# Kernel tuning notes

Hardware: AMD Instinct MI355X
Metric: run time of the kernel (lower is better)

Reference implementation:

```python
import jax, jax.numpy as jnp
import numpy as np

B, S, D = 2, 4096, 768
H, HD = 12, 64  # num_head, head_dim


def setup_inputs() -> dict:
    key = jax.random.key(0)
    ks = jax.random.split(key, 10)
    s = 0.02
    return {
        "X": jax.random.normal(ks[0], (B, S, D), dtype=jnp.float32),
        "mask": jnp.ones((B, S), dtype=jnp.float32),
        "Wq": jax.random.normal(ks[1], (D, H * HD), dtype=jnp.float32) * s,
        "bq": jnp.zeros((H * HD,), dtype=jnp.float32),
        "Wk": jax.random.normal(ks[2], (D, H * HD), dtype=jnp.float32) * s,
        "bk": jnp.zeros((H * HD,), dtype=jnp.float32),
        "Wv": jax.random.normal(ks[3], (D, H * HD), dtype=jnp.float32) * s,
        "bv": jnp.zeros((H * HD,), dtype=jnp.float32),
        "Wo": jax.random.normal(ks[4], (H * HD, D), dtype=jnp.float32) * s,
        "bo": jnp.zeros((D,), dtype=jnp.float32),
    }


def _split_heads(x):
    # [B,S,H*HD] -> [B,H,S,HD]
    return x.reshape(B, S, H, HD).transpose(0, 2, 1, 3)


def reference(X, mask, Wq, bq, Wk, bk, Wv, bv, Wo, bo):
    Q = _split_heads(X @ Wq + bq)
    K = _split_heads(X @ Wk + bk)
    V = _split_heads(X @ Wv + bv)
    # scores: [B,H,S,S]
    dot = jnp.einsum("bhqd,bhkd->bhqk", Q, K) / np.sqrt(HD).astype(np.float32)
    dot = dot - 1e6 * (1.0 - mask[:, None, None, :])
    attn = jax.nn.softmax(dot, axis=-1)
    ctx = jnp.einsum("bhqk,bhkd->bhqd", attn, V)
    # combine heads: [B,H,S,HD] -> [B,S,H*HD]
    ctx = ctx.transpose(0, 2, 1, 3).reshape(B, S, H * HD)
    return ctx @ Wo + bo
```

## Files before the change

### kernel.cpp

```cpp
#include <hip/hip_runtime.h>

#define BATCH   2
#define S_LEN   4096
#define D_MODEL 768
#define NH      12
#define HDIM    64
#define MROWS   (BATCH * S_LEN)
#define QBLK    128
#define KVBLK   64
#define NT      (S_LEN / KVBLK)
#define LOG2E   1.4426950408889634f

typedef float f32x4  __attribute__((ext_vector_type(4)));
typedef float f32x16 __attribute__((ext_vector_type(16)));
typedef short bf16x8 __attribute__((ext_vector_type(8)));

#if __has_builtin(__builtin_amdgcn_exp2f)
#define EXP2(x) __builtin_amdgcn_exp2f(x)
#else
#define EXP2(x) exp2f(x)
#endif

static __device__ __forceinline__ unsigned short f2bf(float f) {
  union { float f; unsigned u; } v; v.f = f;
  unsigned r = v.u + 0x7fffu + ((v.u >> 16) & 1u);
  return (unsigned short)(r >> 16);
}

static __device__ __forceinline__ unsigned cvtpk(float lo, float hi) {
  unsigned r;
  asm("v_cvt_pk_bf16_f32 %0, %1, %2" : "=v"(r) : "v"(lo), "v"(hi));
  return r;
}

typedef __attribute__((address_space(1))) const unsigned int as1_cuint;
typedef __attribute__((address_space(3))) unsigned int as3_uint;
static __device__ __forceinline__ void gload_lds16(const unsigned short* g,
                                                   unsigned short* l) {
  __builtin_amdgcn_global_load_lds((as1_cuint*)g, (as3_uint*)l, 16, 0, 0);
}

template <int BASE>
static __device__ __forceinline__ bf16x8 pack_frag(const f32x16& s) {
  unsigned a0 = cvtpk(s[BASE + 0], s[BASE + 1]);
  unsigned b0 = cvtpk(s[BASE + 4], s[BASE + 5]);
  asm("v_permlane32_swap_b32 %0, %1" : "+v"(a0), "+v"(b0));
  unsigned a1 = cvtpk(s[BASE + 2], s[BASE + 3]);
  unsigned b1 = cvtpk(s[BASE + 6], s[BASE + 7]);
  asm("v_permlane32_swap_b32 %0, %1" : "+v"(a1), "+v"(b1));
  union { unsigned w[4]; bf16x8 v; } u;
  u.w[0] = a0; u.w[1] = a1; u.w[2] = b0; u.w[3] = b1;
  return u.v;
}

#define Z16 {0.f,0.f,0.f,0.f,0.f,0.f,0.f,0.f,0.f,0.f,0.f,0.f,0.f,0.f,0.f,0.f}


__global__ void conv_x(const float* __restrict__ X, unsigned short* __restrict__ Xb) {
  int i = blockIdx.x * blockDim.x + threadIdx.x;
  float4 v = ((const float4*)X)[i];
  ushort4 o;
  o.x = f2bf(v.x); o.y = f2bf(v.y); o.z = f2bf(v.z); o.w = f2bf(v.w);
  ((ushort4*)Xb)[i] = o;
}

__global__ __launch_bounds__(1024) void mask_prep(const float* __restrict__ mask,
                                                  float* __restrict__ madd,
                                                  int* __restrict__ flag) {
  __shared__ int ok[16];
  int t = threadIdx.x;
  int all1 = 1;
  #pragma unroll
  for (int i = 0; i < MROWS / 1024; ++i) {
    int idx = i * 1024 + t;
    float m = mask[idx];
    madd[idx] = (-1e6f * LOG2E) * (1.0f - m);
    all1 &= (m == 1.0f);
  }
  all1 = __all(all1) ? 1 : 0;
  if ((t & 63) == 0) ok[t >> 6] = all1;
  __syncthreads();
  if (t == 0) {
    int a = 1;
    #pragma unroll
    for (int i = 0; i < 16; ++i) a &= ok[i];
    *flag = a;
  }
}

__global__ __launch_bounds__(256) void trans_w(
    const float* __restrict__ W0, const float* __restrict__ W1,
    const float* __restrict__ W2, const float* __restrict__ W3,
    unsigned short* __restrict__ T0, unsigned short* __restrict__ T1,
    unsigned short* __restrict__ T2, unsigned short* __restrict__ T3) {
  const float* W; unsigned short* T;
  int zz = blockIdx.z;
  if (zz == 0) { W = W0; T = T0; }
  else if (zz == 1) { W = W1; T = T1; }
  else if (zz == 2) { W = W2; T = T2; }
  else { W = W3; T = T3; }
  __shared__ float tile[32][33];
  int tx = threadIdx.x & 31, ty = threadIdx.x >> 5;
  int bx = blockIdx.x * 32, by = blockIdx.y * 32;
  #pragma unroll
  for (int i = ty; i < 32; i += 8) tile[i][tx] = W[(size_t)(by + i) * D_MODEL + bx + tx];
  __syncthreads();
  #pragma unroll
  for (int i = ty; i < 32; i += 8)
    T[(size_t)(bx + i) * D_MODEL + by + tx] = f2bf(tile[tx][i]);
}

__global__ __launch_bounds__(256) void qkv_gemm(
    const unsigned short* __restrict__ Xb,
    const unsigned short* __restrict__ Wqt, const unsigned short* __restrict__ Wkt,
    const unsigned short* __restrict__ Wvt,
    const float* __restrict__ bq, const float* __restrict__ bk, const float* __restrict__ bv,
    unsigned short* __restrict__ Qo, unsigned short* __restrict__ Ko,
    unsigned short* __restrict__ Vto) {
  __shared__ unsigned short As[128 * 64];
  __shared__ unsigned short Bs[128 * 64];
  int zz = blockIdx.z;
  const unsigned short* Wt = zz == 0 ? Wqt : (zz == 1 ? Wkt : Wvt);
  const float* bias = zz == 0 ? bq : (zz == 1 ? bk : bv);
  int tid = threadIdx.x;
  int w = tid >> 6, lane = tid & 63, lr = lane & 15, lg = lane >> 4;
  int wr = w >> 1, wc = w & 1;
  int mb = blockIdx.x * 128, nb = blockIdx.y * 128;
  const unsigned short* Ag = Xb + (size_t)(mb + (tid >> 3)) * D_MODEL + (tid & 7) * 8;
  const unsigned short* Bg = Wt + (size_t)(nb + (tid >> 3)) * D_MODEL + (tid & 7) * 8;
  unsigned short* Al = As + (size_t)tid * 8;
  unsigned short* Bl = Bs + (size_t)tid * 8;
  f32x4 acc[4][4];
  #pragma unroll
  for (int m = 0; m < 4; ++m)
    #pragma unroll
    for (int n = 0; n < 4; ++n) acc[m][n] = (f32x4){0.f, 0.f, 0.f, 0.f};
  for (int kb = 0; kb < D_MODEL / 64; ++kb) {
    __syncthreads();
    #pragma unroll
    for (int i = 0; i < 4; ++i) {
      gload_lds16(Ag + (size_t)(i * 32) * D_MODEL + kb * 64, Al + i * 2048);
      gload_lds16(Bg + (size_t)(i * 32) * D_MODEL + kb * 64, Bl + i * 2048);
    }
    __syncthreads();
    #pragma unroll
    for (int kk = 0; kk < 2; ++kk) {
      bf16x8 af[4], bfv[4];
      #pragma unroll
      for (int m = 0; m < 4; ++m)
        af[m] = *(const bf16x8*)(As + (wr * 64 + m * 16 + lr) * 64 + kk * 32 + lg * 8);
      #pragma unroll
      for (int n = 0; n < 4; ++n)
        bfv[n] = *(const bf16x8*)(Bs + (wc * 64 + n * 16 + lr) * 64 + kk * 32 + lg * 8);
      #pragma unroll
      for (int m = 0; m < 4; ++m)
        #pragma unroll
        for (int n = 0; n < 4; ++n)
          acc[m][n] = __builtin_amdgcn_mfma_f32_16x16x32_bf16(af[m], bfv[n], acc[m][n], 0, 0, 0);
    }
  }
  #pragma unroll
  for (int n = 0; n < 4; ++n) {
    int nc = nb + wc * 64 + n * 16 + lr;
    float bia = bias[nc];
    int h = nc >> 6, hd = nc & 63;
    #pragma unroll
    for (int m = 0; m < 4; ++m) {
      #pragma unroll
      for (int r = 0; r < 4; ++r) {
        int mr = mb + wr * 64 + m * 16 + lg * 4 + r;
        int b = mr >> 12, s = mr & 4095;
        float val = acc[m][n][r] + bia;
        if (zz == 0)
          Qo[((size_t)(b * NH + h) * S_LEN + s) * HDIM + hd] = f2bf(val * 0.125f * LOG2E);
        else if (zz == 1)
          Ko[((size_t)(b * NH + h) * S_LEN + s) * HDIM + hd] = f2bf(val);
        else
          Vto[((size_t)(b * NH + h) * HDIM + hd) * S_LEN + s] = f2bf(val);
      }
    }
  }
}

__global__ __launch_bounds__(256) void attn_kernel(
    const unsigned short* __restrict__ Q, const unsigned short* __restrict__ K,
    const unsigned short* __restrict__ Vt, const float* __restrict__ madd,
    const int* __restrict__ allones_p, unsigned short* __restrict__ Ctx) {
  __shared__ unsigned short Ks[2][64][72];
  __shared__ unsigned short Vs[2][64][72];
  int lin = blockIdx.x;
  int wg = (lin & 7) * 96 + (lin >> 3);
  int qb = wg & 31, bh = wg >> 5;
  int b = bh / NH, h = bh % NH;
  int tid = threadIdx.x;
  int w = tid >> 6, lane = tid & 63;
  int lq = lane & 31, hi = lane >> 5;
  const unsigned short* Qb = Q + (size_t)bh * S_LEN * HDIM;
  const unsigned short* Kb = K + (size_t)bh * S_LEN * HDIM;
  const unsigned short* Vb = Vt + (size_t)bh * HDIM * S_LEN;
  const float* maddb = madd + (size_t)b * S_LEN;
  const int allones = *allones_p;

  int qrow = qb * QBLK + w * 32 + lq;
  bf16x8 qf0 = *(const bf16x8*)(Qb + (size_t)qrow * HDIM + 0 * 16 + hi * 8);
  bf16x8 qf1 = *(const bf16x8*)(Qb + (size_t)qrow * HDIM + 1 * 16 + hi * 8);
  bf16x8 qf2 = *(const bf16x8*)(Qb + (size_t)qrow * HDIM + 2 * 16 + hi * 8);
  bf16x8 qf3 = *(const bf16x8*)(Qb + (size_t)qrow * HDIM + 3 * 16 + hi * 8);

  f32x16 acc0 = Z16, acc1 = Z16;
  float l_run = 0.f;

  int srow = tid >> 3, sseg = (tid & 7) * 8;
  uint4 ka, kc, va, vc;

  ka = *(const uint4*)(Kb + (size_t)srow * HDIM + sseg);
  kc = *(const uint4*)(Kb + (size_t)(srow + 32) * HDIM + sseg);
  va = *(const uint4*)(Vb + (size_t)srow * S_LEN + sseg);
  vc = *(const uint4*)(Vb + (size_t)(srow + 32) * S_LEN + sseg);
  *(uint4*)&Ks[0][srow][sseg]      = ka;
  *(uint4*)&Ks[0][srow + 32][sseg] = kc;
  *(uint4*)&Vs[0][srow][sseg]      = va;
  *(uint4*)&Vs[0][srow + 32][sseg] = vc;
  __syncthreads();

  for (int t = 0; t < NT; ++t) {
    int cur = t & 1;
    int kbase = t * KVBLK;
    if (t + 1 < NT) {
      int nb2 = kbase + KVBLK;
      ka = *(const uint4*)(Kb + (size_t)(nb2 + srow) * HDIM + sseg);
      kc = *(const uint4*)(Kb + (size_t)(nb2 + srow + 32) * HDIM + sseg);
      va = *(const uint4*)(Vb + (size_t)srow * S_LEN + nb2 + sseg);
      vc = *(const uint4*)(Vb + (size_t)(srow + 32) * S_LEN + nb2 + sseg);
    }
    f32x16 s0 = Z16, s1 = Z16;
    #pragma unroll
    for (int c = 0; c < 4; ++c) {
      bf16x8 kf0 = *(const bf16x8*)(&Ks[cur][lq][c * 16 + hi * 8]);
      bf16x8 kf1 = *(const bf16x8*)(&Ks[cur][32 + lq][c * 16 + hi * 8]);
      bf16x8 qf = c == 0 ? qf0 : (c == 1 ? qf1 : (c == 2 ? qf2 : qf3));
      s0 = __builtin_amdgcn_mfma_f32_32x32x16_bf16(kf0, qf, s0, 0, 0, 0);
      s1 = __builtin_amdgcn_mfma_f32_32x32x16_bf16(kf1, qf, s1, 0, 0, 0);
    }
    if (!allones) {
      #pragma unroll
      for (int g = 0; g < 4; ++g) {
        float4 m0 = *(const float4*)(maddb + kbase + g * 8 + hi * 4);
        float4 m1 = *(const float4*)(maddb + kbase + 32 + g * 8 + hi * 4);
        s0[g * 4 + 0] += m0.x; s0[g * 4 + 1] += m0.y;
        s0[g * 4 + 2] += m0.z; s0[g * 4 + 3] += m0.w;
        s1[g * 4 + 0] += m1.x; s1[g * 4 + 1] += m1.y;
        s1[g * 4 + 2] += m1.z; s1[g * 4 + 3] += m1.w;
      }
    }
    float psA = 0.f, psB = 0.f, psC = 0.f, psD = 0.f;
    #pragma unroll
    for (int r = 0; r < 4; ++r) {
      s0[r]      = EXP2(s0[r]);      psA += s0[r];
      s0[r + 4]  = EXP2(s0[r + 4]);  psB += s0[r + 4];
      s0[r + 8]  = EXP2(s0[r + 8]);  psC += s0[r + 8];
      s0[r + 12] = EXP2(s0[r + 12]); psD += s0[r + 12];
    }
    #pragma unroll
    for (int r = 0; r < 4; ++r) {
      s1[r]      = EXP2(s1[r]);      psA += s1[r];
      s1[r + 4]  = EXP2(s1[r + 4]);  psB += s1[r + 4];
      s1[r + 8]  = EXP2(s1[r + 8]);  psC += s1[r + 8];
      s1[r + 12] = EXP2(s1[r + 12]); psD += s1[r + 12];
    }
    float psum = (psA + psB) + (psC + psD);
    psum += __shfl_xor(psum, 32, 64);
    l_run += psum;
    bf16x8 pa0 = pack_frag<0>(s0);
    bf16x8 pa1 = pack_frag<8>(s0);
    bf16x8 pa2 = pack_frag<0>(s1);
    bf16x8 pa3 = pack_frag<8>(s1);
    #pragma unroll
    for (int c = 0; c < 4; ++c) {
      bf16x8 pa = c == 0 ? pa0 : (c == 1 ? pa1 : (c == 2 ? pa2 : pa3));
      bf16x8 vf0 = *(const bf16x8*)(&Vs[cur][lq][c * 16 + hi * 8]);
      bf16x8 vf1 = *(const bf16x8*)(&Vs[cur][32 + lq][c * 16 + hi * 8]);
      acc0 = __builtin_amdgcn_mfma_f32_32x32x16_bf16(pa, vf0, acc0, 0, 0, 0);
      acc1 = __builtin_amdgcn_mfma_f32_32x32x16_bf16(pa, vf1, acc1, 0, 0, 0);
    }
    if (t + 1 < NT) {
      int nxt = cur ^ 1;
      *(uint4*)&Ks[nxt][srow][sseg]      = ka;
      *(uint4*)&Ks[nxt][srow + 32][sseg] = kc;
      *(uint4*)&Vs[nxt][srow][sseg]      = va;
      *(uint4*)&Vs[nxt][srow + 32][sseg] = vc;
      __syncthreads();
    }
  }
  #pragma unroll
  for (int r = 0; r < 16; ++r) {
    int qr = (r & 3) + 8 * (r >> 2) + 4 * hi;
    float lv = __shfl(l_run, qr, 64);
    float rl = 1.0f / lv;
    int qglob = qb * QBLK + w * 32 + qr;
    size_t base = ((size_t)(b * S_LEN + qglob)) * D_MODEL + h * HDIM;
    Ctx[base + lq]      = f2bf(acc0[r] * rl);
    Ctx[base + 32 + lq] = f2bf(acc1[r] * rl);
  }
}

__global__ __launch_bounds__(256) void out_gemm(
    const unsigned short* __restrict__ Ctx, const unsigned short* __restrict__ Wot,
    const float* __restrict__ bo, float* __restrict__ Out) {
  __shared__ unsigned short As[128 * 64];
  __shared__ unsigned short Bs[128 * 64];
  int tid = threadIdx.x;
  int w = tid >> 6, lane = tid & 63, lr = lane & 15, lg = lane >> 4;
  int wr = w >> 1, wc = w & 1;
  int mb = blockIdx.x * 128, nb = blockIdx.y * 128;
  const unsigned short* Ag = Ctx + (size_t)(mb + (tid >> 3)) * D_MODEL + (tid & 7) * 8;
  const unsigned short* Bg = Wot + (size_t)(nb + (tid >> 3)) * D_MODEL + (tid & 7) * 8;
  unsigned short* Al = As + (size_t)tid * 8;
  unsigned short* Bl = Bs + (size_t)tid * 8;
  f32x4 acc[4][4];
  #pragma unroll
  for (int m = 0; m < 4; ++m)
    #pragma unroll
    for (int n = 0; n < 4; ++n) acc[m][n] = (f32x4){0.f, 0.f, 0.f, 0.f};
  for (int kb = 0; kb < D_MODEL / 64; ++kb) {
    __syncthreads();
    #pragma unroll
    for (int i = 0; i < 4; ++i) {
      gload_lds16(Ag + (size_t)(i * 32) * D_MODEL + kb * 64, Al + i * 2048);
      gload_lds16(Bg + (size_t)(i * 32) * D_MODEL + kb * 64, Bl + i * 2048);
    }
    __syncthreads();
    #pragma unroll
    for (int kk = 0; kk < 2; ++kk) {
      bf16x8 af[4], bfv[4];
      #pragma unroll
      for (int m = 0; m < 4; ++m)
        af[m] = *(const bf16x8*)(As + (wr * 64 + m * 16 + lr) * 64 + kk * 32 + lg * 8);
      #pragma unroll
      for (int n = 0; n < 4; ++n)
        bfv[n] = *(const bf16x8*)(Bs + (wc * 64 + n * 16 + lr) * 64 + kk * 32 + lg * 8);
      #pragma unroll
      for (int m = 0; m < 4; ++m)
        #pragma unroll
        for (int n = 0; n < 4; ++n)
          acc[m][n] = __builtin_amdgcn_mfma_f32_16x16x32_bf16(af[m], bfv[n], acc[m][n], 0, 0, 0);
    }
  }
  #pragma unroll
  for (int n = 0; n < 4; ++n) {
    int nc = nb + wc * 64 + n * 16 + lr;
    float bia = bo[nc];
    #pragma unroll
    for (int m = 0; m < 4; ++m) {
      #pragma unroll
      for (int r = 0; r < 4; ++r) {
        int mr = mb + wr * 64 + m * 16 + lg * 4 + r;
        Out[(size_t)mr * D_MODEL + nc] = acc[m][n][r] + bia;
      }
    }
  }
}


extern "C" void kernel_launch(void* const* d_in, const int* in_sizes, int n_in,
                              void* d_out, int out_size, void* d_ws, size_t ws_size,
                              hipStream_t stream) {
  const float* X    = (const float*)d_in[0];
  const float* mask = (const float*)d_in[1];
  const float* Wq   = (const float*)d_in[2];
  const float* bq   = (const float*)d_in[3];
  const float* Wk   = (const float*)d_in[4];
  const float* bk   = (const float*)d_in[5];
  const float* Wv   = (const float*)d_in[6];
  const float* bv   = (const float*)d_in[7];
  const float* Wo   = (const float*)d_in[8];
  const float* bo   = (const float*)d_in[9];
  float* out = (float*)d_out;
  char* ws = (char*)d_ws;

  const size_t XB_OFF   = 0;
  const size_t WQT_OFF  = 12582912;
  const size_t WKT_OFF  = WQT_OFF + 1179648;
  const size_t WVT_OFF  = WKT_OFF + 1179648;
  const size_t WOT_OFF  = WVT_OFF + 1179648;
  const size_t Q_OFF    = WOT_OFF + 1179648;
  const size_t K_OFF    = Q_OFF + 12582912;
  const size_t VT_OFF   = K_OFF + 12582912;
  const size_t CTX_OFF  = VT_OFF + 12582912;
  const size_t MADD_OFF = CTX_OFF + 12582912;
  const size_t FLAG_OFF = MADD_OFF + MROWS * 4;

  unsigned short* Xb  = (unsigned short*)(ws + XB_OFF);
  unsigned short* Wqt = (unsigned short*)(ws + WQT_OFF);
  unsigned short* Wkt = (unsigned short*)(ws + WKT_OFF);
  unsigned short* Wvt = (unsigned short*)(ws + WVT_OFF);
  unsigned short* Wot = (unsigned short*)(ws + WOT_OFF);
  unsigned short* Qw  = (unsigned short*)(ws + Q_OFF);
  unsigned short* Kw  = (unsigned short*)(ws + K_OFF);
  unsigned short* Vtw = (unsigned short*)(ws + VT_OFF);
  unsigned short* Ctx = (unsigned short*)(ws + CTX_OFF);
  float* madd = (float*)(ws + MADD_OFF);
  int* flag   = (int*)(ws + FLAG_OFF);

  conv_x<<<dim3(MROWS * D_MODEL / 4 / 256), 256, 0, stream>>>(X, Xb);
  mask_prep<<<dim3(1), 1024, 0, stream>>>(mask, madd, flag);
  trans_w<<<dim3(24, 24, 4), 256, 0, stream>>>(Wq, Wk, Wv, Wo, Wqt, Wkt, Wvt, Wot);
  qkv_gemm<<<dim3(MROWS / 128, D_MODEL / 128, 3), 256, 0, stream>>>(
      Xb, Wqt, Wkt, Wvt, bq, bk, bv, Qw, Kw, Vtw);
  attn_kernel<<<dim3((S_LEN / QBLK) * (BATCH * NH)), 256, 0, stream>>>(
      Qw, Kw, Vtw, madd, flag, Ctx);
  out_gemm<<<dim3(MROWS / 128, D_MODEL / 128), 256, 0, stream>>>(Ctx, Wot, bo, out);
}
```

Measured before the change: 257.6 us.

## Split attention KV range in two halves and merge with combine kernel

Splits each attention workgroup's KV sweep into two halves processed by separate workgroups, doubling the grid from 768 to 1536 blocks. Each half writes unnormalized bf16 partial outputs and row sums, and a new combine kernel adds the partials and divides by the summed denominators. The aim is better occupancy and load balance across the GPU's compute units. In exchange it adds an extra kernel launch, extra global traffic, and extra bf16 rounding of unnormalized partials, and it reuses the Xb and weight-transpose buffers as scratch. It relies on the absence of a running max, so partial sums add directly.

New measurement: 260.7 us. About the same (+1.2%).

```diff
diff --git a/kernel.cpp b/kernel.cpp
--- a/kernel.cpp
+++ b/kernel.cpp
@@ -8,7 +8,8 @@
 #define MROWS   (BATCH * S_LEN)
 #define QBLK    128
 #define KVBLK   64
-#define NT      (S_LEN / KVBLK)
+#define KVHALF  2048
+#define NTH     (KVHALF / KVBLK)
 #define LOG2E   1.4426950408889634f
 
 typedef float f32x4  __attribute__((ext_vector_type(4)));
@@ -25,6 +26,10 @@
   union { float f; unsigned u; } v; v.f = f;
   unsigned r = v.u + 0x7fffu + ((v.u >> 16) & 1u);
   return (unsigned short)(r >> 16);
+}
+
+static __device__ __forceinline__ float bf2f(unsigned short u) {
+  union { unsigned u; float f; } v; v.u = ((unsigned)u) << 16; return v.f;
 }
 
 static __device__ __forceinline__ unsigned cvtpk(float lo, float hi) {
@@ -185,12 +190,17 @@
 __global__ __launch_bounds__(256) void attn_kernel(
     const unsigned short* __restrict__ Q, const unsigned short* __restrict__ K,
     const unsigned short* __restrict__ Vt, const float* __restrict__ madd,
-    const int* __restrict__ allones_p, unsigned short* __restrict__ Ctx) {
+    const int* __restrict__ allones_p,
+    unsigned short* __restrict__ OutA, unsigned short* __restrict__ OutB,
+    float* __restrict__ lA, float* __restrict__ lB) {
   __shared__ unsigned short Ks[2][64][72];
   __shared__ unsigned short Vs[2][64][72];
   int lin = blockIdx.x;
-  int wg = (lin & 7) * 96 + (lin >> 3);
-  int qb = wg & 31, bh = wg >> 5;
+  int wg = (lin & 7) * 192 + (lin >> 3);
+  int bh = wg >> 6;
+  int rem = wg & 63;
+  int half = rem & 1;
+  int qb = rem >> 1;
   int b = bh / NH, h = bh % NH;
   int tid = threadIdx.x;
   int w = tid >> 6, lane = tid & 63;
@@ -200,6 +210,8 @@
   const unsigned short* Vb = Vt + (size_t)bh * HDIM * S_LEN;
   const float* maddb = madd + (size_t)b * S_LEN;
   const int allones = *allones_p;
+  unsigned short* outp = half ? OutB : OutA;
+  float* lp = half ? lB : lA;
 
   int qrow = qb * QBLK + w * 32 + lq;
   bf16x8 qf0 = *(const bf16x8*)(Qb + (size_t)qrow * HDIM + 0 * 16 + hi * 8);
@@ -211,22 +223,23 @@
   float l_run = 0.f;
 
   int srow = tid >> 3, sseg = (tid & 7) * 8;
+  int kv0 = half * KVHALF;
   uint4 ka, kc, va, vc;
 
-  ka = *(const uint4*)(Kb + (size_t)srow * HDIM + sseg);
-  kc = *(const uint4*)(Kb + (size_t)(srow + 32) * HDIM + sseg);
-  va = *(const uint4*)(Vb + (size_t)srow * S_LEN + sseg);
-  vc = *(const uint4*)(Vb + (size_t)(srow + 32) * S_LEN + sseg);
+  ka = *(const uint4*)(Kb + (size_t)(kv0 + srow) * HDIM + sseg);
+  kc = *(const uint4*)(Kb + (size_t)(kv0 + srow + 32) * HDIM + sseg);
+  va = *(const uint4*)(Vb + (size_t)srow * S_LEN + kv0 + sseg);
+  vc = *(const uint4*)(Vb + (size_t)(srow + 32) * S_LEN + kv0 + sseg);
   *(uint4*)&Ks[0][srow][sseg]      = ka;
   *(uint4*)&Ks[0][srow + 32][sseg] = kc;
   *(uint4*)&Vs[0][srow][sseg]      = va;
   *(uint4*)&Vs[0][srow + 32][sseg] = vc;
   __syncthreads();
 
-  for (int t = 0; t < NT; ++t) {
+  for (int t = 0; t < NTH; ++t) {
     int cur = t & 1;
-    int kbase = t * KVBLK;
-    if (t + 1 < NT) {
+    int kbase = kv0 + t * KVBLK;
+    if (t + 1 < NTH) {
       int nb2 = kbase + KVBLK;
       ka = *(const uint4*)(Kb + (size_t)(nb2 + srow) * HDIM + sseg);
       kc = *(const uint4*)(Kb + (size_t)(nb2 + srow + 32) * HDIM + sseg);
@@ -283,7 +296,7 @@
       acc0 = __builtin_amdgcn_mfma_f32_32x32x16_bf16(pa, vf0, acc0, 0, 0, 0);
       acc1 = __builtin_amdgcn_mfma_f32_32x32x16_bf16(pa, vf1, acc1, 0, 0, 0);
     }
-    if (t + 1 < NT) {
+    if (t + 1 < NTH) {
       int nxt = cur ^ 1;
       *(uint4*)&Ks[nxt][srow][sseg]      = ka;
       *(uint4*)&Ks[nxt][srow + 32][sseg] = kc;
@@ -295,13 +308,39 @@
   #pragma unroll
   for (int r = 0; r < 16; ++r) {
     int qr = (r & 3) + 8 * (r >> 2) + 4 * hi;
-    float lv = __shfl(l_run, qr, 64);
-    float rl = 1.0f / lv;
     int qglob = qb * QBLK + w * 32 + qr;
     size_t base = ((size_t)(b * S_LEN + qglob)) * D_MODEL + h * HDIM;
-    Ctx[base + lq]      = f2bf(acc0[r] * rl);
-    Ctx[base + 32 + lq] = f2bf(acc1[r] * rl);
-  }
+    outp[base + lq]      = f2bf(acc0[r]);
+    outp[base + 32 + lq] = f2bf(acc1[r]);
+  }
+  if (hi == 0)
+    lp[(size_t)bh * S_LEN + qb * QBLK + w * 32 + lq] = l_run;
+}
+
+__global__ __launch_bounds__(256) void combine(
+    const unsigned short* __restrict__ OB, const float* __restrict__ lA,
+    const float* __restrict__ lB, unsigned short* __restrict__ OA) {
+  int bh = blockIdx.y, b = bh / NH, h = bh % NH;
+  int t = threadIdx.x;
+  int s = blockIdx.x * 32 + (t >> 3);
+  int d = (t & 7) * 8;
+  float rl = 1.0f / (lA[(size_t)bh * S_LEN + s] + lB[(size_t)bh * S_LEN + s]);
+  size_t idx = ((size_t)(b * S_LEN + s)) * D_MODEL + h * HDIM + d;
+  ushort4 a0 = *(const ushort4*)(OA + idx);
+  ushort4 a1 = *(const ushort4*)(OA + idx + 4);
+  ushort4 b0 = *(const ushort4*)(OB + idx);
+  ushort4 b1 = *(const ushort4*)(OB + idx + 4);
+  ushort4 o0, o1;
+  o0.x = f2bf((bf2f(a0.x) + bf2f(b0.x)) * rl);
+  o0.y = f2bf((bf2f(a0.y) + bf2f(b0.y)) * rl);
+  o0.z = f2bf((bf2f(a0.z) + bf2f(b0.z)) * rl);
+  o0.w = f2bf((bf2f(a0.w) + bf2f(b0.w)) * rl);
+  o1.x = f2bf((bf2f(a1.x) + bf2f(b1.x)) * rl);
+  o1.y = f2bf((bf2f(a1.y) + bf2f(b1.y)) * rl);
+  o1.z = f2bf((bf2f(a1.z) + bf2f(b1.z)) * rl);
+  o1.w = f2bf((bf2f(a1.w) + bf2f(b1.w)) * rl);
+  *(ushort4*)(OA + idx)     = o0;
+  *(ushort4*)(OA + idx + 4) = o1;
 }
 
 __global__ __launch_bounds__(256) void out_gemm(
@@ -401,13 +440,17 @@
   unsigned short* Ctx = (unsigned short*)(ws + CTX_OFF);
   float* madd = (float*)(ws + MADD_OFF);
   int* flag   = (int*)(ws + FLAG_OFF);
+  unsigned short* OutB = Xb;
+  float* lA = (float*)(ws + WQT_OFF);
+  float* lB = (float*)(ws + WKT_OFF);
 
   conv_x<<<dim3(MROWS * D_MODEL / 4 / 256), 256, 0, stream>>>(X, Xb);
   mask_prep<<<dim3(1), 1024, 0, stream>>>(mask, madd, flag);
   trans_w<<<dim3(24, 24, 4), 256, 0, stream>>>(Wq, Wk, Wv, Wo, Wqt, Wkt, Wvt, Wot);
   qkv_gemm<<<dim3(MROWS / 128, D_MODEL / 128, 3), 256, 0, stream>>>(
       Xb, Wqt, Wkt, Wvt, bq, bk, bv, Qw, Kw, Vtw);
-  attn_kernel<<<dim3((S_LEN / QBLK) * (BATCH * NH)), 256, 0, stream>>>(
-      Qw, Kw, Vtw, madd, flag, Ctx);
+  attn_kernel<<<dim3((S_LEN / QBLK) * (BATCH * NH) * 2), 256, 0, stream>>>(
+      Qw, Kw, Vtw, madd, flag, Ctx, OutB, lA, lB);
+  combine<<<dim3(S_LEN / 32, BATCH * NH), 256, 0, stream>>>(OutB, lA, lB, Ctx);
   out_gemm<<<dim3(MROWS / 128, D_MODEL / 128), 256, 0, stream>>>(Ctx, Wot, bo, out);
 }
```
